# Optimization experiments

Hardware: AMD Instinct MI355X
Metric: run time of the kernel (lower is better)

Reference implementation:

```python
import jax, jax.numpy as jnp
import numpy as np

B, N, D = 2, 256, 512
H = 4 * D  # mlp_hidden_dim


def setup_inputs() -> dict:
    key = jax.random.key(0)
    ks = jax.random.split(key, 14)
    s_in = 1.0 / np.sqrt(D)
    s_h = 1.0 / np.sqrt(H)
    s_cat = 1.0 / np.sqrt(2 * D)
    return {
        "x_v": jax.random.normal(ks[0], (B, N, D), jnp.float32),
        "x_a": jax.random.normal(ks[1], (B, N, D), jnp.float32),
        # weights stored as (in, out); y = x @ W + b (same math as torch Linear)
        "W1v": jax.random.uniform(ks[2], (D, H), jnp.float32, -s_in, s_in),
        "b1v": jax.random.uniform(ks[3], (H,), jnp.float32, -s_in, s_in),
        "W1a": jax.random.uniform(ks[4], (D, H), jnp.float32, -s_in, s_in),
        "b1a": jax.random.uniform(ks[5], (H,), jnp.float32, -s_in, s_in),
        "Wmv": jax.random.uniform(ks[6], (H, D), jnp.float32, -s_h, s_h),
        "bmv": jax.random.uniform(ks[7], (D,), jnp.float32, -s_h, s_h),
        "Wma": jax.random.uniform(ks[8], (H, D), jnp.float32, -s_h, s_h),
        "bma": jax.random.uniform(ks[9], (D,), jnp.float32, -s_h, s_h),
        "Wout": jax.random.uniform(ks[10], (2 * D, D), jnp.float32, -s_cat, s_cat),
        "bout": jax.random.uniform(ks[11], (D,), jnp.float32, -s_cat, s_cat),
    }


def reference(x_v, x_a, W1v, b1v, W1a, b1a, Wmv, bmv, Wma, bma, Wout, bout):
    # pairwise Manhattan distance: [B, N, M]
    dist = jnp.sum(jnp.abs(x_v[:, :, None, :] - x_a[:, None, :, :]), axis=-1)
    dv = dist.mean(axis=2)  # [B, N] mean distance of each v-token to all a-tokens
    da = dist.mean(axis=1)  # [B, M]
    xv_w = x_v * dv[..., None]
    xa_w = x_a * da[..., None]
    # dropout prob = 0.0 -> identity
    hv = jax.nn.gelu(xv_w @ W1v + b1v, approximate=False) @ Wmv + bmv
    ha = jax.nn.gelu(xa_w @ W1a + b1a, approximate=False) @ Wma + bma
    combined = jnp.concatenate([hv, ha], axis=-1)  # [B, N, 2D]
    return combined @ Wout + bout
```

## Files before the change

### kernel.cpp

```cpp
#include <hip/hip_runtime.h>
#include <math.h>

#define Bsz  2
#define Ntok 256
#define Ddim 512
#define Hdim 2048
#define Mrows 512

typedef __bf16 bf16_8 __attribute__((ext_vector_type(8)));
typedef __bf16 bf16_4 __attribute__((ext_vector_type(4)));
typedef __bf16 bf16_2 __attribute__((ext_vector_type(2)));
typedef float  f32x4_t __attribute__((ext_vector_type(4)));

struct PrepPtrs {
    const float* src[3];
    __bf16*      dst[3];
    const float* xv;
    const float* xa;
    __bf16*      xbf[2];
    float*       pv;
    float*       pa;
    const float* bm[2];
    const float* Wout;
    const float* bout;
    float*       bc;
    float*       outz;
};

__global__ __launch_bounds__(256) void prep_kernel(PrepPtrs p) {
    __shared__ float tile[64][65];
    __shared__ float red[4][8];

    int blk = blockIdx.x;
    int tid = threadIdx.x;

    if (blk < 640) {
        const int Ks[3]  = {512, 512, 1024};
        const int Ns[3]  = {2048, 2048, 512};
        const int off[4] = {0, 256, 512, 640};
        int mi = 0;
        while (blk >= off[mi + 1]) ++mi;
        int local = blk - off[mi];
        int shift = (mi < 2) ? 5 : 3;
        int bx = local & ((1 << shift) - 1);
        int by = local >> shift;
        const float* src = p.src[mi];
        __bf16*      dst = p.dst[mi];
        int K = Ks[mi], N = Ns[mi];
        int n0 = bx << 6, k0 = by << 6;

        int klb = tid >> 4, nl = (tid & 15) << 2;
#pragma unroll
        for (int pass = 0; pass < 4; ++pass) {
            int kl = (pass << 4) + klb;
            float4 v = *(const float4*)&src[(size_t)(k0 + kl) * N + n0 + nl];
            tile[kl][nl + 0] = v.x;
            tile[kl][nl + 1] = v.y;
            tile[kl][nl + 2] = v.z;
            tile[kl][nl + 3] = v.w;
        }
        __syncthreads();
        int nl2 = tid >> 2, kb = (tid & 3) << 2;
#pragma unroll
        for (int pass = 0; pass < 4; ++pass) {
            int kl2 = (pass << 4) + kb;
            bf16_4 o;
#pragma unroll
            for (int i = 0; i < 4; ++i) o[i] = (__bf16)tile[kl2 + i][nl2];
            *(bf16_4*)&dst[(size_t)(n0 + nl2) * K + k0 + kl2] = o;
        }
    } else if (blk < 1152) {
        int bx   = blk - 640;
        int jc   = bx & 3;
        int g    = bx >> 2;
        int role = g >> 6;
        int b    = (g >> 5) & 1;
        int i0   = (g & 31) << 3;
        const float* Q    = role ? p.xa : p.xv;
        const float* S    = role ? p.xv : p.xa;
        float*       outp = role ? p.pa : p.pv;

        int d0 = tid << 1;
        const float* Qb = Q + ((size_t)b * Ntok + i0) * Ddim + d0;
        const float* Sb = S + ((size_t)b * Ntok + (jc << 6)) * Ddim + d0;

        float2 q[8];
#pragma unroll
        for (int r = 0; r < 8; ++r) q[r] = *(const float2*)(Qb + r * Ddim);

        if (jc == 0) {
            __bf16* xb = p.xbf[role];
#pragma unroll
            for (int r = 0; r < 8; ++r) {
                bf16_2 o;
                o[0] = (__bf16)q[r].x;
                o[1] = (__bf16)q[r].y;
                *(bf16_2*)&xb[((size_t)b * Ntok + i0 + r) * Ddim + d0] = o;
            }
        }

        float acc[8] = {0.f, 0.f, 0.f, 0.f, 0.f, 0.f, 0.f, 0.f};
#pragma unroll 2
        for (int j = 0; j < 64; ++j) {
            float2 s = *(const float2*)(Sb + (size_t)j * Ddim);
#pragma unroll
            for (int r = 0; r < 8; ++r)
                acc[r] += fabsf(q[r].x - s.x) + fabsf(q[r].y - s.y);
        }
        int lane = tid & 63, wv = tid >> 6;
#pragma unroll
        for (int r = 0; r < 8; ++r) {
            float v = acc[r];
#pragma unroll
            for (int off2 = 32; off2; off2 >>= 1) v += __shfl_down(v, off2);
            if (lane == 0) red[wv][r] = v;
        }
        __syncthreads();
        if (tid < 8) {
            float v = red[0][tid] + red[1][tid] + red[2][tid] + red[3][tid];
            outp[jc * Mrows + b * Ntok + i0 + tid] = v;
        }
    } else if (blk < 1160) {
        int kb = blk - 1152;
        float a0 = 0.f, a1 = 0.f, a2 = 0.f, a3 = 0.f;
#pragma unroll 4
        for (int kk = 0; kk < 128; kk += 2) {
            int k0 = (kb << 7) + kk, k1 = k0 + 1;
            float bk0 = (k0 < 512) ? p.bm[0][k0] : p.bm[1][k0 - 512];
            float bk1 = (k1 < 512) ? p.bm[0][k1] : p.bm[1][k1 - 512];
            a0 += bk0 * p.Wout[(size_t)k0 * Ddim + tid];
            a1 += bk0 * p.Wout[(size_t)k0 * Ddim + tid + 256];
            a2 += bk1 * p.Wout[(size_t)k1 * Ddim + tid];
            a3 += bk1 * p.Wout[(size_t)k1 * Ddim + tid + 256];
        }
        if (kb == 0) { a0 += p.bout[tid]; a1 += p.bout[tid + 256]; }
        p.bc[(kb << 9) + tid]       = a0 + a2;
        p.bc[(kb << 9) + tid + 256] = a1 + a3;
    } else {
        int ib = blk - 1160;
        float4 z4 = {0.f, 0.f, 0.f, 0.f};
        float4* o = (float4*)p.outz + (size_t)ib * 1024 + tid;
#pragma unroll
        for (int pass = 0; pass < 4; ++pass) o[pass * 256] = z4;
    }
}

template <int GELU, int AMODE, int BFP32, int OUTM>
__device__ void gemm_tile(__bf16 (&As)[2][64][40], __bf16 (&Bs)[2][64][40],
                          const void* Aa, int lda, const void* Bv, int ldb,
                          const float* bias, const float* scale4,
                          void* C, int ldc, int Kdim,
                          int m0, int n0, int addBias) {
    const int tid = threadIdx.x;
    const int row = tid >> 2;
    const int kc  = (tid & 3) << 3;

    const __bf16* Bb  = (const __bf16*)Bv + (size_t)(n0 + row) * ldb + kc;
    const float*  Bf  = (const float*)Bv + (size_t)(n0 + row) * ldb + kc;
    const float*  Af  = (const float*)Aa + (size_t)(m0 + row) * lda + kc;
    const __bf16* Ab  = (const __bf16*)Aa + (size_t)(m0 + row) * lda + kc;
    float s = 1.0f;
    if (AMODE == 1 || AMODE == 3) {
        int m = m0 + row;
        s = (scale4[m] + scale4[Mrows + m] + scale4[2 * Mrows + m] +
             scale4[3 * Mrows + m]) * (1.0f / 256.0f);
    }

    const int wave = tid >> 6, lane = tid & 63;
    const int moff = (wave >> 1) << 5, noff = (wave & 1) << 5;
    const int lrow = lane & 15, quad = lane >> 4;

    struct Stage {
        float4 aF0, aF1, bF0, bF1;
        bf16_8 a8, b8;
    };
    Stage sR, sN;

    auto loadStage = [&](int kt, Stage& st) {
        if (BFP32) {
            st.bF0 = *(const float4*)(Bf + kt);
            st.bF1 = *(const float4*)(Bf + kt + 4);
        } else {
            st.b8 = *(const bf16_8*)(Bb + kt);
        }
        if (AMODE == 1) {
            st.aF0 = *(const float4*)(Af + kt);
            st.aF1 = *(const float4*)(Af + kt + 4);
        } else {
            st.a8 = *(const bf16_8*)(Ab + kt);
        }
    };
    auto storeStage = [&](int buf, const Stage& st) {
        bf16_8 a8, b8;
        if (AMODE == 1) {
            a8[0] = (__bf16)(st.aF0.x * s); a8[1] = (__bf16)(st.aF0.y * s);
            a8[2] = (__bf16)(st.aF0.z * s); a8[3] = (__bf16)(st.aF0.w * s);
            a8[4] = (__bf16)(st.aF1.x * s); a8[5] = (__bf16)(st.aF1.y * s);
            a8[6] = (__bf16)(st.aF1.z * s); a8[7] = (__bf16)(st.aF1.w * s);
        } else if (AMODE == 3) {
#pragma unroll
            for (int i = 0; i < 8; ++i)
                a8[i] = (__bf16)((float)st.a8[i] * s);
        } else {
            a8 = st.a8;
        }
        if (BFP32) {
            b8[0] = (__bf16)st.bF0.x; b8[1] = (__bf16)st.bF0.y;
            b8[2] = (__bf16)st.bF0.z; b8[3] = (__bf16)st.bF0.w;
            b8[4] = (__bf16)st.bF1.x; b8[5] = (__bf16)st.bF1.y;
            b8[6] = (__bf16)st.bF1.z; b8[7] = (__bf16)st.bF1.w;
        } else {
            b8 = st.b8;
        }
        *(bf16_8*)&As[buf][row][kc] = a8;
        *(bf16_8*)&Bs[buf][row][kc] = b8;
    };

    f32x4_t acc00 = {0.f, 0.f, 0.f, 0.f};
    f32x4_t acc01 = {0.f, 0.f, 0.f, 0.f};
    f32x4_t acc10 = {0.f, 0.f, 0.f, 0.f};
    f32x4_t acc11 = {0.f, 0.f, 0.f, 0.f};

    const int nIter = Kdim >> 5;

    loadStage(0, sR);
    storeStage(0, sR);
    if (nIter > 1) loadStage(32, sR);
    __syncthreads();

    for (int it = 0; it < nIter; ++it) {
        const int cur = it & 1;
        bf16_8 a0 = *(const bf16_8*)&As[cur][moff + lrow][quad << 3];
        bf16_8 a1 = *(const bf16_8*)&As[cur][moff + 16 + lrow][quad << 3];
        bf16_8 b0 = *(const bf16_8*)&Bs[cur][noff + lrow][quad << 3];
        bf16_8 b1 = *(const bf16_8*)&Bs[cur][noff + 16 + lrow][quad << 3];
        if (it + 2 < nIter) loadStage((it + 2) << 5, sN);
        acc00 = __builtin_amdgcn_mfma_f32_16x16x32_bf16(a0, b0, acc00, 0, 0, 0);
        acc01 = __builtin_amdgcn_mfma_f32_16x16x32_bf16(a0, b1, acc01, 0, 0, 0);
        acc10 = __builtin_amdgcn_mfma_f32_16x16x32_bf16(a1, b0, acc10, 0, 0, 0);
        acc11 = __builtin_amdgcn_mfma_f32_16x16x32_bf16(a1, b1, acc11, 0, 0, 0);
        if (it + 1 < nIter) {
            storeStage(cur ^ 1, sR);
            sR = sN;
            __syncthreads();
        }
    }

    f32x4_t accs[2][2] = {{acc00, acc01}, {acc10, acc11}};
#pragma unroll
    for (int ti = 0; ti < 2; ++ti) {
#pragma unroll
        for (int tj = 0; tj < 2; ++tj) {
            int colg = n0 + noff + (tj << 4) + lrow;
            float bv = 0.0f;
            if (addBias == 1) {
                bv = bias[colg];
            } else if (addBias == 2) {
#pragma unroll
                for (int k = 0; k < 8; ++k) bv += bias[(k << 9) + colg];
            }
#pragma unroll
            for (int r = 0; r < 4; ++r) {
                int rowg = m0 + moff + (ti << 4) + (quad << 2) + r;
                float v = accs[ti][tj][r] + bv;
                if (GELU) v = 0.5f * v * (1.0f + erff(v * 0.70710678118654752f));
                if (OUTM == 1)
                    ((__bf16*)C)[(size_t)rowg * ldc + colg] = (__bf16)v;
                else
                    atomicAdd((float*)C + (size_t)rowg * ldc + colg, v);
            }
        }
    }
}

struct APtrs {
    const __bf16* xbf[2];
    const __bf16* WT1[2];
    const float*  b1[2];
    const float*  pd[2];
    __bf16*       g1[2];
    const __bf16* WTout;
    const float*  Wm[2];
    __bf16*       WcT[2];
};

__global__ __launch_bounds__(256) void kernelA(APtrs p) {
    __shared__ __align__(16) __bf16 As[2][64][40];
    __shared__ __align__(16) __bf16 Bs[2][64][40];
    int blk = blockIdx.x;
    if (blk < 512) {
        int z = blk >> 8, t = blk & 255;
        int mt = t >> 5, nt = t & 31;
        gemm_tile<1, 3, 0, 1>(As, Bs, p.xbf[z], Ddim, p.WT1[z], Ddim,
                              p.b1[z], p.pd[z], p.g1[z], Hdim, Ddim,
                              mt << 6, nt << 6, 1);
    } else {
        int b2 = blk - 512;
        int z = b2 >> 8, t = b2 & 255;
        int mt = t >> 5, nt = t & 31;
        gemm_tile<0, 0, 1, 1>(As, Bs, p.WTout + z * 512, 2 * Ddim,
                              p.Wm[z], Ddim, nullptr, nullptr,
                              p.WcT[z], Hdim, Ddim, mt << 6, nt << 6, 0);
    }
}

struct BPtrs {
    const __bf16* g1[2];
    const __bf16* WcT[2];
    const float*  bc;
    float*        out;
};

__global__ __launch_bounds__(256) void kernelB(BPtrs p) {
    __shared__ __align__(16) __bf16 As[2][64][40];
    __shared__ __align__(16) __bf16 Bs[2][64][40];
    int nt = blockIdx.x & 7, mt = (blockIdx.x >> 3) & 7, kz = blockIdx.x >> 6;
    int z = kz >> 1, koff = (kz & 1) << 10;
    gemm_tile<0, 0, 0, 2>(As, Bs, p.g1[z] + koff, Hdim, p.WcT[z] + koff, Hdim,
                          p.bc, nullptr, p.out, Ddim, 1024,
                          mt << 6, nt << 6, kz == 0 ? 2 : 0);
}

extern "C" void kernel_launch(void* const* d_in, const int* in_sizes, int n_in,
                              void* d_out, int out_size, void* d_ws, size_t ws_size,
                              hipStream_t stream) {
    const float* x_v  = (const float*)d_in[0];
    const float* x_a  = (const float*)d_in[1];
    const float* W1v  = (const float*)d_in[2];
    const float* b1v  = (const float*)d_in[3];
    const float* W1a  = (const float*)d_in[4];
    const float* b1a  = (const float*)d_in[5];
    const float* Wmv  = (const float*)d_in[6];
    const float* bmv  = (const float*)d_in[7];
    const float* Wma  = (const float*)d_in[8];
    const float* bma  = (const float*)d_in[9];
    const float* Wout = (const float*)d_in[10];
    const float* bout = (const float*)d_in[11];
    float* out = (float*)d_out;

    char* w = (char*)d_ws;
    auto alloc = [&](size_t bytes) {
        char* r = w;
        w += (bytes + 255) & ~(size_t)255;
        return (void*)r;
    };
    float*    pv    = (float*)alloc(4 * Mrows * 4);
    float*    pa    = (float*)alloc(4 * Mrows * 4);
    float*    bc    = (float*)alloc(8 * Ddim * 4);
    __bf16*   xbfv  = (__bf16*)alloc((size_t)Mrows * Ddim * 2);
    __bf16*   xbfa  = (__bf16*)alloc((size_t)Mrows * Ddim * 2);
    __bf16*   WT1v  = (__bf16*)alloc((size_t)Hdim * Ddim * 2);
    __bf16*   WT1a  = (__bf16*)alloc((size_t)Hdim * Ddim * 2);
    __bf16*   WTout = (__bf16*)alloc((size_t)Ddim * 2 * Ddim * 2);
    __bf16*   WcTv  = (__bf16*)alloc((size_t)Ddim * Hdim * 2);
    __bf16*   WcTa  = (__bf16*)alloc((size_t)Ddim * Hdim * 2);
    __bf16*   g1v   = (__bf16*)alloc((size_t)Mrows * Hdim * 2);
    __bf16*   g1a   = (__bf16*)alloc((size_t)Mrows * Hdim * 2);

    PrepPtrs pp;
    pp.src[0] = W1v;  pp.dst[0] = WT1v;
    pp.src[1] = W1a;  pp.dst[1] = WT1a;
    pp.src[2] = Wout; pp.dst[2] = WTout;
    pp.xv = x_v; pp.xa = x_a;
    pp.xbf[0] = xbfv; pp.xbf[1] = xbfa;
    pp.pv = pv; pp.pa = pa;
    pp.bm[0] = bmv; pp.bm[1] = bma;
    pp.Wout = Wout; pp.bout = bout;
    pp.bc = bc;
    pp.outz = out;
    prep_kernel<<<dim3(1224), dim3(256), 0, stream>>>(pp);

    APtrs ap;
    ap.xbf[0] = xbfv; ap.xbf[1] = xbfa;
    ap.WT1[0] = WT1v; ap.WT1[1] = WT1a;
    ap.b1[0] = b1v; ap.b1[1] = b1a;
    ap.pd[0] = pv; ap.pd[1] = pa;
    ap.g1[0] = g1v; ap.g1[1] = g1a;
    ap.WTout = WTout;
    ap.Wm[0] = Wmv; ap.Wm[1] = Wma;
    ap.WcT[0] = WcTv; ap.WcT[1] = WcTa;
    kernelA<<<dim3(1024), dim3(256), 0, stream>>>(ap);

    BPtrs bp;
    bp.g1[0] = g1v; bp.g1[1] = g1a;
    bp.WcT[0] = WcTv; bp.WcT[1] = WcTa;
    bp.bc = bc; bp.out = out;
    kernelB<<<dim3(256), dim3(256), 0, stream>>>(bp);
}
```

Measured before the change: 128.4 us.

## Fuse GEMM kernels A and B with atomic counter barrier; read fp32 x directly

Kernels A and B are merged into a single launch. The last 256 blocks spin on a global counter until all 1024 first-stage blocks have signalled completion, then run the second GEMM. Separately, the bf16 copy of x in the prep kernel is dropped, and the first GEMM now loads fp32 x directly through a different A-mode template. This removes one kernel launch boundary and one intermediate buffer write, but the spin-wait blocks occupy compute slots and depend on forward progress, and converting fp32 inside the GEMM may cost extra load bandwidth.

```diff
diff --git a/kernel.cpp b/kernel.cpp
--- a/kernel.cpp
+++ b/kernel.cpp
@@ -17,7 +17,6 @@
     __bf16*      dst[3];
     const float* xv;
     const float* xa;
-    __bf16*      xbf[2];
     float*       pv;
     float*       pa;
     const float* bm[2];
@@ -25,6 +24,7 @@
     const float* bout;
     float*       bc;
     float*       outz;
+    int*         cnt;
 };
 
 __global__ __launch_bounds__(256) void prep_kernel(PrepPtrs p) {
@@ -88,17 +88,6 @@
 #pragma unroll
         for (int r = 0; r < 8; ++r) q[r] = *(const float2*)(Qb + r * Ddim);
 
-        if (jc == 0) {
-            __bf16* xb = p.xbf[role];
-#pragma unroll
-            for (int r = 0; r < 8; ++r) {
-                bf16_2 o;
-                o[0] = (__bf16)q[r].x;
-                o[1] = (__bf16)q[r].y;
-                *(bf16_2*)&xb[((size_t)b * Ntok + i0 + r) * Ddim + d0] = o;
-            }
-        }
-
         float acc[8] = {0.f, 0.f, 0.f, 0.f, 0.f, 0.f, 0.f, 0.f};
 #pragma unroll 2
         for (int j = 0; j < 64; ++j) {
@@ -138,6 +127,7 @@
         p.bc[(kb << 9) + tid + 256] = a1 + a3;
     } else {
         int ib = blk - 1160;
+        if (ib == 0 && tid == 0) *p.cnt = 0;
         float4 z4 = {0.f, 0.f, 0.f, 0.f};
         float4* o = (float4*)p.outz + (size_t)ib * 1024 + tid;
 #pragma unroll
@@ -273,8 +263,8 @@
     }
 }
 
-struct APtrs {
-    const __bf16* xbf[2];
+struct ABPtrs {
+    const float*  x[2];
     const __bf16* WT1[2];
     const float*  b1[2];
     const float*  pd[2];
@@ -282,43 +272,50 @@
     const __bf16* WTout;
     const float*  Wm[2];
     __bf16*       WcT[2];
+    const float*  bc;
+    float*        out;
+    int*          cnt;
 };
 
-__global__ __launch_bounds__(256) void kernelA(APtrs p) {
+__global__ __launch_bounds__(256) void kernelAB(ABPtrs p) {
     __shared__ __align__(16) __bf16 As[2][64][40];
     __shared__ __align__(16) __bf16 Bs[2][64][40];
     int blk = blockIdx.x;
-    if (blk < 512) {
-        int z = blk >> 8, t = blk & 255;
-        int mt = t >> 5, nt = t & 31;
-        gemm_tile<1, 3, 0, 1>(As, Bs, p.xbf[z], Ddim, p.WT1[z], Ddim,
-                              p.b1[z], p.pd[z], p.g1[z], Hdim, Ddim,
-                              mt << 6, nt << 6, 1);
+    int tid = threadIdx.x;
+    if (blk < 1024) {
+        if (blk < 512) {
+            int z = blk >> 8, t = blk & 255;
+            int mt = t >> 5, nt = t & 31;
+            gemm_tile<1, 1, 0, 1>(As, Bs, p.x[z], Ddim, p.WT1[z], Ddim,
+                                  p.b1[z], p.pd[z], p.g1[z], Hdim, Ddim,
+                                  mt << 6, nt << 6, 1);
+        } else {
+            int b2 = blk - 512;
+            int z = b2 >> 8, t = b2 & 255;
+            int mt = t >> 5, nt = t & 31;
+            gemm_tile<0, 0, 1, 1>(As, Bs, p.WTout + z * 512, 2 * Ddim,
+                                  p.Wm[z], Ddim, nullptr, nullptr,
+                                  p.WcT[z], Hdim, Ddim, mt << 6, nt << 6, 0);
+        }
+        __syncthreads();
+        if (tid == 0)
+            __hip_atomic_fetch_add(p.cnt, 1, __ATOMIC_RELEASE,
+                                   __HIP_MEMORY_SCOPE_AGENT);
     } else {
-        int b2 = blk - 512;
-        int z = b2 >> 8, t = b2 & 255;
-        int mt = t >> 5, nt = t & 31;
-        gemm_tile<0, 0, 1, 1>(As, Bs, p.WTout + z * 512, 2 * Ddim,
-                              p.Wm[z], Ddim, nullptr, nullptr,
-                              p.WcT[z], Hdim, Ddim, mt << 6, nt << 6, 0);
-    }
-}
-
-struct BPtrs {
-    const __bf16* g1[2];
-    const __bf16* WcT[2];
-    const float*  bc;
-    float*        out;
-};
-
-__global__ __launch_bounds__(256) void kernelB(BPtrs p) {
-    __shared__ __align__(16) __bf16 As[2][64][40];
-    __shared__ __align__(16) __bf16 Bs[2][64][40];
-    int nt = blockIdx.x & 7, mt = (blockIdx.x >> 3) & 7, kz = blockIdx.x >> 6;
-    int z = kz >> 1, koff = (kz & 1) << 10;
-    gemm_tile<0, 0, 0, 2>(As, Bs, p.g1[z] + koff, Hdim, p.WcT[z] + koff, Hdim,
-                          p.bc, nullptr, p.out, Ddim, 1024,
-                          mt << 6, nt << 6, kz == 0 ? 2 : 0);
+        if (tid == 0) {
+            while (__hip_atomic_load(p.cnt, __ATOMIC_ACQUIRE,
+                                     __HIP_MEMORY_SCOPE_AGENT) < 1024)
+                __builtin_amdgcn_s_sleep(16);
+        }
+        __syncthreads();
+        int bk = blk - 1024;
+        int nt = bk & 7, mt = (bk >> 3) & 7, kz = bk >> 6;
+        int z = kz >> 1, koff = (kz & 1) << 10;
+        gemm_tile<0, 0, 0, 2>(As, Bs, p.g1[z] + koff, Hdim,
+                              p.WcT[z] + koff, Hdim,
+                              p.bc, nullptr, p.out, Ddim, 1024,
+                              mt << 6, nt << 6, kz == 0 ? 2 : 0);
+    }
 }
 
 extern "C" void kernel_launch(void* const* d_in, const int* in_sizes, int n_in,
@@ -347,8 +344,7 @@
     float*    pv    = (float*)alloc(4 * Mrows * 4);
     float*    pa    = (float*)alloc(4 * Mrows * 4);
     float*    bc    = (float*)alloc(8 * Ddim * 4);
-    __bf16*   xbfv  = (__bf16*)alloc((size_t)Mrows * Ddim * 2);
-    __bf16*   xbfa  = (__bf16*)alloc((size_t)Mrows * Ddim * 2);
+    int*      cnt   = (int*)alloc(256);
     __bf16*   WT1v  = (__bf16*)alloc((size_t)Hdim * Ddim * 2);
     __bf16*   WT1a  = (__bf16*)alloc((size_t)Hdim * Ddim * 2);
     __bf16*   WTout = (__bf16*)alloc((size_t)Ddim * 2 * Ddim * 2);
@@ -362,28 +358,24 @@
     pp.src[1] = W1a;  pp.dst[1] = WT1a;
     pp.src[2] = Wout; pp.dst[2] = WTout;
     pp.xv = x_v; pp.xa = x_a;
-    pp.xbf[0] = xbfv; pp.xbf[1] = xbfa;
     pp.pv = pv; pp.pa = pa;
     pp.bm[0] = bmv; pp.bm[1] = bma;
     pp.Wout = Wout; pp.bout = bout;
     pp.bc = bc;
     pp.outz = out;
+    pp.cnt = cnt;
     prep_kernel<<<dim3(1224), dim3(256), 0, stream>>>(pp);
 
-    APtrs ap;
-    ap.xbf[0] = xbfv; ap.xbf[1] = xbfa;
-    ap.WT1[0] = WT1v; ap.WT1[1] = WT1a;
-    ap.b1[0] = b1v; ap.b1[1] = b1a;
-    ap.pd[0] = pv; ap.pd[1] = pa;
-    ap.g1[0] = g1v; ap.g1[1] = g1a;
-    ap.WTout = WTout;
-    ap.Wm[0] = Wmv; ap.Wm[1] = Wma;
-    ap.WcT[0] = WcTv; ap.WcT[1] = WcTa;
-    kernelA<<<dim3(1024), dim3(256), 0, stream>>>(ap);
-
-    BPtrs bp;
-    bp.g1[0] = g1v; bp.g1[1] = g1a;
-    bp.WcT[0] = WcTv; bp.WcT[1] = WcTa;
-    bp.bc = bc; bp.out = out;
-    kernelB<<<dim3(256), dim3(256), 0, stream>>>(bp);
+    ABPtrs ab;
+    ab.x[0] = x_v; ab.x[1] = x_a;
+    ab.WT1[0] = WT1v; ab.WT1[1] = WT1a;
+    ab.b1[0] = b1v; ab.b1[1] = b1a;
+    ab.pd[0] = pv; ab.pd[1] = pa;
+    ab.g1[0] = g1v; ab.g1[1] = g1a;
+    ab.WTout = WTout;
+    ab.Wm[0] = Wmv; ab.Wm[1] = Wma;
+    ab.WcT[0] = WcTv; ab.WcT[1] = WcTa;
+    ab.bc = bc; ab.out = out;
+    ab.cnt = cnt;
+    kernelAB<<<dim3(1280), dim3(256), 0, stream>>>(ab);
 }
```

Result: slower. 213.8 us (+66.5%).
